# Performance work log

Measured on AMD Instinct MI355X. Metric: run time of the kernel, lower is better.

Reference implementation:

```python
import jax, jax.numpy as jnp
import numpy as np

B, T, D = 2, 2048, 2048
H, LAT, RD = 16, 512, 64
HD = D // H  # 128


def _rope_tables(rd, max_t, theta=10000.0):
    freqs = 1.0 / theta ** (np.arange(0, rd, 2, dtype=np.float32) / rd)
    t = np.arange(max_t, dtype=np.float32)
    ang = np.outer(t, freqs)                      # (T, rd/2)
    cos = np.tile(np.cos(ang), (1, 2))            # (T, rd), matches torch .repeat(1,2)
    sin = np.tile(np.sin(ang), (1, 2))
    return jnp.asarray(cos), jnp.asarray(sin)


def _rotate_half(x):
    d = x.shape[-1] // 2
    return jnp.concatenate([-x[..., d:], x[..., :d]], axis=-1)


def _apply_rope(x, cos, sin):
    # x: (B, H, T, rd); cos/sin: (T, rd) broadcast over B, H
    t = x.shape[2]
    return x * cos[:t][None, None] + _rotate_half(x) * sin[:t][None, None]


def setup_inputs() -> dict:
    key = jax.random.key(0)
    ks = jax.random.split(key, 9)
    s = 0.02  # init scale to keep logits sane
    return {
        "x": jax.random.normal(ks[0], (B, T, D), jnp.float32),
        "Wqd": jax.random.normal(ks[1], (D, LAT), jnp.float32) * s,
        "Wqu": jax.random.normal(ks[2], (LAT, D), jnp.float32) * s,
        "Wqr": jax.random.normal(ks[3], (LAT, H * RD), jnp.float32) * s,
        "Wkvd": jax.random.normal(ks[4], (D, LAT), jnp.float32) * s,
        "Wku": jax.random.normal(ks[5], (LAT, D), jnp.float32) * s,
        "Wvu": jax.random.normal(ks[6], (LAT, D), jnp.float32) * s,
        "Wkr": jax.random.normal(ks[7], (D, RD), jnp.float32) * s,
        "Wo": jax.random.normal(ks[8], (D, D), jnp.float32) * s,
    }


def reference(x, Wqd, Wqu, Wqr, Wkvd, Wku, Wvu, Wkr, Wo):
    b, t, d = x.shape
    cos, sin = _rope_tables(RD, t)

    ql = x @ Wqd                                            # (B,T,LAT)
    q = (ql @ Wqu).reshape(b, t, H, HD).transpose(0, 2, 1, 3)      # (B,H,T,hd)
    qr = (ql @ Wqr).reshape(b, t, H, RD).transpose(0, 2, 1, 3)     # (B,H,T,rd)
    qr = _apply_rope(qr, cos, sin)

    ckv = x @ Wkvd                                          # (B,T,LAT)
    k = (ckv @ Wku).reshape(b, t, H, HD).transpose(0, 2, 1, 3)     # (B,H,T,hd)
    v = (ckv @ Wvu).reshape(b, t, H, HD).transpose(0, 2, 1, 3)     # (B,H,T,hd)

    kr = _apply_rope((x @ Wkr)[:, None], cos, sin)[:, 0]    # (B,T,rd), shared over heads

    scale = 1.0 / jnp.sqrt(jnp.float32(HD + RD))
    scores = (jnp.einsum('bhtd,bhsd->bhts', q, k)
              + jnp.einsum('bhtd,bsd->bhts', qr, kr)) * scale       # (B,H,T,T)

    causal = jnp.tril(jnp.ones((t, t), dtype=bool))
    scores = jnp.where(causal[None, None], scores, jnp.float32(-jnp.inf))
    attn = jax.nn.softmax(scores, axis=-1)

    out = jnp.einsum('bhts,bhsd->bhtd', attn, v)            # (B,H,T,hd)
    out = out.transpose(0, 2, 1, 3).reshape(b, t, d)        # (B,T,D)
    return out @ Wo
```

## Files before the change

kernel.cpp:

```cpp
#include <hip/hip_runtime.h>
#include <cmath>

typedef unsigned short ushort;
typedef __bf16 bf16x8 __attribute__((ext_vector_type(8)));
typedef float f32x4 __attribute__((ext_vector_type(4)));
typedef float f32x16 __attribute__((ext_vector_type(16)));
typedef unsigned int uint4v __attribute__((ext_vector_type(4)));
typedef unsigned int u2v __attribute__((ext_vector_type(2)));
typedef unsigned short ushort4v __attribute__((ext_vector_type(4)));

#define BB 2
#define TT 2048
#define DD 2048
#define HH 16
#define LATD 512
#define RDD 64
#define HDD 128
#define BT 4096
#define LDQ 2048
#define LDK 4096
#define LD1 1088

__device__ __forceinline__ ushort f2bf(float f) {
  union { float f; unsigned u; } v; v.f = f;
  return (ushort)((v.u + 0x7fffu + ((v.u >> 16) & 1u)) >> 16);
}
__device__ __forceinline__ float bf2f(ushort u) {
  union { unsigned u; float f; } v; v.u = ((unsigned)u) << 16; return v.f;
}
__device__ __forceinline__ f32x4 f4zero() {
  f32x4 v; v[0] = 0.f; v[1] = 0.f; v[2] = 0.f; v[3] = 0.f; return v;
}
__device__ __forceinline__ unsigned pkbf(float a, float b) {
  unsigned r;
  asm("v_cvt_pk_bf16_f32 %0, %1, %2" : "=v"(r) : "v"(a), "v"(b));
  return r;
}
__device__ __forceinline__ u2v pl32(unsigned a, unsigned b) {
  return __builtin_amdgcn_permlane32_swap(a, b, false, false);
}
__device__ __forceinline__ float xswap32(float v, int hl) {
  union { float f; unsigned u; } a; a.f = v;
  u2v r = pl32(a.u, a.u);
  union { unsigned u; float f; } o; o.u = hl ? r[0] : r[1];
  return o.f;
}

typedef __attribute__((address_space(1))) void g_void;
typedef __attribute__((address_space(3))) void l_void;
__device__ __forceinline__ void gld16(void* lds, const void* g) {
  __builtin_amdgcn_global_load_lds((g_void*)(unsigned long long)g, (l_void*)lds, 16, 0, 0);
}

__global__ void k_cvt(const float* __restrict__ in, ushort* __restrict__ out, int n4) {
  int i = blockIdx.x * 256 + threadIdx.x;
  if (i >= n4) return;
  f32x4 v = *(const f32x4*)(in + (size_t)i * 4);
  ushort4v u;
#pragma unroll
  for (int r = 0; r < 4; ++r) u[r] = f2bf(v[r]);
  *(ushort4v*)(out + (size_t)i * 4) = u;
}

__global__ void k_twall(const float* __restrict__ Wqd, const float* __restrict__ Wkvd,
                        const float* __restrict__ Wkr, const float* __restrict__ Wqu,
                        const float* __restrict__ Wqr, const float* __restrict__ Wku,
                        const float* __restrict__ Wvu, const float* __restrict__ Wo,
                        ushort* __restrict__ w1T, ushort* __restrict__ w2T,
                        ushort* __restrict__ w3T, ushort* __restrict__ woT) {
  __shared__ float t[32][33];
  int bid = blockIdx.x;
  const float* in; ushort* out; int R, C, gx;
  if (bid < 1024)      { in = Wqd;  out = w1T;                          R = 2048; C = 512;  gx = 16; }
  else if (bid < 2048) { in = Wkvd; out = w1T + (size_t)512 * 2048;     R = 2048; C = 512;  gx = 16; bid -= 1024; }
  else if (bid < 2176) { in = Wkr;  out = w1T + (size_t)1024 * 2048;    R = 2048; C = 64;   gx = 2;  bid -= 2048; }
  else if (bid < 3200) { in = Wqu;  out = w2T;                          R = 512;  C = 2048; gx = 64; bid -= 2176; }
  else if (bid < 3712) { in = Wqr;  out = w2T + (size_t)2048 * 512;     R = 512;  C = 1024; gx = 32; bid -= 3200; }
  else if (bid < 4736) { in = Wku;  out = w3T;                          R = 512;  C = 2048; gx = 64; bid -= 3712; }
  else if (bid < 5760) { in = Wvu;  out = w3T + (size_t)2048 * 512;     R = 512;  C = 2048; gx = 64; bid -= 4736; }
  else                 { in = Wo;   out = woT;                          R = 2048; C = 2048; gx = 64; bid -= 5760; }
  int c0 = (bid % gx) * 32, r0 = (bid / gx) * 32;
  int tx = threadIdx.x, ty = threadIdx.y;
#pragma unroll
  for (int i = 0; i < 4; ++i)
    t[ty + i * 8][tx] = in[(size_t)(r0 + ty + i * 8) * C + c0 + tx];
  __syncthreads();
#pragma unroll
  for (int i = 0; i < 4; ++i)
    out[(size_t)(c0 + ty + i * 8) * R + r0 + tx] = f2bf(t[tx][ty + i * 8]);
}

__global__ void k_tables(float* __restrict__ cosT, float* __restrict__ sinT) {
  int i = blockIdx.x * 256 + threadIdx.x;
  int t = i >> 5, jj = i & 31;
  float freq = exp2f(-(float)jj * (13.287712379549449f / 32.0f));
  float ang = (float)t * freq;
  float s, c;
  sincosf(ang, &s, &c);
  cosT[i] = c; sinT[i] = s;
}

__global__ void k_rope(const ushort* __restrict__ in, int in_stride, ushort* __restrict__ out,
                       int lw, const float* __restrict__ cosT, const float* __restrict__ sinT) {
  int idx = blockIdx.x * 256 + threadIdx.x;
  int row = idx >> lw, col = idx & ((1 << lw) - 1);
  int t = row & (TT - 1);
  int j = col & 63, jj = j & 31;
  float c = cosT[t * 32 + jj], s = sinT[t * 32 + jj];
  const ushort* ip = in + (size_t)row * in_stride;
  float xv = bf2f(ip[col]);
  float xp = (j < 32) ? -bf2f(ip[col + 32]) : bf2f(ip[col - 32]);
  out[idx] = f2bf(xv * c + xp * s);
}

__global__ void k_vt(const ushort* __restrict__ in, ushort* __restrict__ out) {
  __shared__ ushort tile[32][33];
  int bh = blockIdx.z, b = bh >> 4, h = bh & 15;
  int t0 = blockIdx.x * 32, d0 = blockIdx.y * 32;
  int tx = threadIdx.x, ty = threadIdx.y;
#pragma unroll
  for (int i = 0; i < 4; ++i)
    tile[ty + i * 8][tx] = in[(size_t)(b * TT + t0 + ty + i * 8) * LDK + h * HDD + d0 + tx];
  __syncthreads();
#pragma unroll
  for (int i = 0; i < 4; ++i)
    out[(size_t)(bh * HDD + d0 + ty + i * 8) * TT + t0 + tx] = tile[tx][ty + i * 8];
}

__global__ void k_ta(const ushort* __restrict__ in, ushort* __restrict__ out) {
  __shared__ ushort tile[32][33];
  int bh = blockIdx.z, b = bh >> 4, h = bh & 15;
  int t0 = blockIdx.x * 32, d0 = blockIdx.y * 32;
  int tx = threadIdx.x, ty = threadIdx.y;
#pragma unroll
  for (int i = 0; i < 4; ++i)
    tile[ty + i * 8][tx] = in[(size_t)(bh * HDD + d0 + ty + i * 8) * TT + t0 + tx];
  __syncthreads();
#pragma unroll
  for (int i = 0; i < 4; ++i)
    out[(size_t)(b * TT + t0 + ty + i * 8) * DD + h * HDD + d0 + tx] = tile[tx][ty + i * 8];
}

template <typename OutT>
__global__ __launch_bounds__(256) void k_gemm(const ushort* __restrict__ A,
                                              const ushort* __restrict__ Bt,
                                              OutT* __restrict__ C,
                                              int M, int N, int K, int lda, int ldc, float alpha) {
  __shared__ __align__(16) ushort As[128 * 64];
  __shared__ __align__(16) ushort Bs[128 * 64];
  int tid = threadIdx.x;
  int lane = tid & 63, wid = tid >> 6;
  int wm = wid >> 1, wn = wid & 1;
  int lo = lane & 15, hi = lane >> 4;
  int m0 = blockIdx.y * 128, n0 = blockIdx.x * 128;
  int lr = lane >> 3, lc = (lane & 7) * 8;
  f32x4 acc[4][4];
#pragma unroll
  for (int m = 0; m < 4; ++m)
#pragma unroll
    for (int n = 0; n < 4; ++n) acc[m][n] = f4zero();

  for (int k0 = 0; k0 < K; k0 += 64) {
    __syncthreads();
#pragma unroll
    for (int it = 0; it < 4; ++it) {
      int c = wid * 4 + it;
      int row = c * 8 + lr;
      gld16(As + c * 512, A + (size_t)(m0 + row) * lda + k0 + lc);
      gld16(Bs + c * 512, Bt + (size_t)(n0 + row) * K + k0 + lc);
    }
    __syncthreads();
#pragma unroll
    for (int kk = 0; kk < 2; ++kk) {
      bf16x8 af[4], bfr[4];
#pragma unroll
      for (int m = 0; m < 4; ++m)
        af[m] = *(const bf16x8*)(As + (wm * 64 + m * 16 + lo) * 64 + kk * 32 + hi * 8);
#pragma unroll
      for (int n = 0; n < 4; ++n)
        bfr[n] = *(const bf16x8*)(Bs + (wn * 64 + n * 16 + lo) * 64 + kk * 32 + hi * 8);
      __builtin_amdgcn_s_setprio(1);
#pragma unroll
      for (int m = 0; m < 4; ++m)
#pragma unroll
        for (int n = 0; n < 4; ++n)
          acc[m][n] = __builtin_amdgcn_mfma_f32_16x16x32_bf16(af[m], bfr[n], acc[m][n], 0, 0, 0);
      __builtin_amdgcn_s_setprio(0);
    }
  }
#pragma unroll
  for (int m = 0; m < 4; ++m)
#pragma unroll
    for (int n = 0; n < 4; ++n)
#pragma unroll
      for (int r = 0; r < 4; ++r) {
        int row = m0 + wm * 64 + m * 16 + hi * 4 + r;
        int col = n0 + wn * 64 + n * 16 + lo;
        if (col < N) {
          float v = acc[m][n][r] * alpha;
          if constexpr (sizeof(OutT) == 4) C[(size_t)row * ldc + col] = v;
          else C[(size_t)row * ldc + col] = f2bf(v);
        }
      }
}

__global__ __launch_bounds__(256) void k_gemm23(const ushort* __restrict__ A1, const ushort* __restrict__ B1,
                                                ushort* __restrict__ Cq, ushort* __restrict__ Cr,
                                                const ushort* __restrict__ A2, const ushort* __restrict__ B2,
                                                ushort* __restrict__ Ckv, float a1,
                                                const float* __restrict__ cosT, const float* __restrict__ sinT) {
  __shared__ __align__(16) ushort As[128 * 64];
  __shared__ __align__(16) ushort Bs[128 * 64];
  int bx = blockIdx.x;
  const ushort* A; const ushort* Bt; int n0;
  if (bx < 24) { A = A1; Bt = B1; n0 = bx * 128; }
  else         { A = A2; Bt = B2; n0 = (bx - 24) * 128; }
  const int K = LATD, lda = LD1;
  int tid = threadIdx.x;
  int lane = tid & 63, wid = tid >> 6;
  int wm = wid >> 1, wn = wid & 1;
  int lo = lane & 15, hi = lane >> 4;
  int m0 = blockIdx.y * 128;
  int lr = lane >> 3, lc = (lane & 7) * 8;
  f32x4 acc[4][4];
#pragma unroll
  for (int m = 0; m < 4; ++m)
#pragma unroll
    for (int n = 0; n < 4; ++n) acc[m][n] = f4zero();

  for (int k0 = 0; k0 < K; k0 += 64) {
    __syncthreads();
#pragma unroll
    for (int it = 0; it < 4; ++it) {
      int c = wid * 4 + it;
      int row = c * 8 + lr;
      gld16(As + c * 512, A + (size_t)(m0 + row) * lda + k0 + lc);
      gld16(Bs + c * 512, Bt + (size_t)(n0 + row) * K + k0 + lc);
    }
    __syncthreads();
#pragma unroll
    for (int kk = 0; kk < 2; ++kk) {
      bf16x8 af[4], bfr[4];
#pragma unroll
      for (int m = 0; m < 4; ++m)
        af[m] = *(const bf16x8*)(As + (wm * 64 + m * 16 + lo) * 64 + kk * 32 + hi * 8);
#pragma unroll
      for (int n = 0; n < 4; ++n)
        bfr[n] = *(const bf16x8*)(Bs + (wn * 64 + n * 16 + lo) * 64 + kk * 32 + hi * 8);
      __builtin_amdgcn_s_setprio(1);
#pragma unroll
      for (int m = 0; m < 4; ++m)
#pragma unroll
        for (int n = 0; n < 4; ++n)
          acc[m][n] = __builtin_amdgcn_mfma_f32_16x16x32_bf16(af[m], bfr[n], acc[m][n], 0, 0, 0);
      __builtin_amdgcn_s_setprio(0);
    }
  }
  if (bx < 16) {
#pragma unroll
    for (int m = 0; m < 4; ++m)
#pragma unroll
      for (int n = 0; n < 4; ++n)
#pragma unroll
        for (int r = 0; r < 4; ++r) {
          int row = m0 + wm * 64 + m * 16 + hi * 4 + r;
          int col = n0 + wn * 64 + n * 16 + lo;
          Cq[(size_t)row * 2048 + col] = f2bf(acc[m][n][r] * a1);
        }
  } else if (bx < 24) {
#pragma unroll
    for (int m = 0; m < 4; ++m)
#pragma unroll
      for (int r = 0; r < 4; ++r) {
        int row = m0 + wm * 64 + m * 16 + hi * 4 + r;
        int t = row & (TT - 1);
        float c0 = cosT[t * 32 + lo],      s0 = sinT[t * 32 + lo];
        float c1 = cosT[t * 32 + 16 + lo], s1 = sinT[t * 32 + 16 + lo];
        float x0 = acc[m][0][r], x1 = acc[m][1][r];
        float x2 = acc[m][2][r], x3 = acc[m][3][r];
        size_t base = (size_t)row * 1024 + (bx - 16) * 128 + wn * 64 + lo;
        Cr[base +  0] = f2bf((x0 * c0 - x2 * s0) * a1);
        Cr[base + 16] = f2bf((x1 * c1 - x3 * s1) * a1);
        Cr[base + 32] = f2bf((x2 * c0 + x0 * s0) * a1);
        Cr[base + 48] = f2bf((x3 * c1 + x1 * s1) * a1);
      }
  } else {
#pragma unroll
    for (int m = 0; m < 4; ++m)
#pragma unroll
      for (int n = 0; n < 4; ++n)
#pragma unroll
        for (int r = 0; r < 4; ++r) {
          int row = m0 + wm * 64 + m * 16 + hi * 4 + r;
          int col = n0 + wn * 64 + n * 16 + lo;
          Ckv[(size_t)row * 4096 + col] = f2bf(acc[m][n][r]);
        }
  }
}

__global__ __launch_bounds__(256, 2) void k_attn(const ushort* __restrict__ qb, const ushort* __restrict__ qrb,
                                                 const ushort* __restrict__ kb, const ushort* __restrict__ krb,
                                                 const ushort* __restrict__ vt, ushort* __restrict__ aoT) {
  __shared__ __align__(16) ushort KsL[2][64 * 128];
  __shared__ __align__(16) ushort KrL[2][64 * 64];
  const int tid = threadIdx.x, lane = tid & 63, w = tid >> 6;
  const int cq = lane & 31;
  const int hl = lane >> 5;
  const int lin = (int)blockIdx.x + 16 * (int)blockIdx.y + 256 * (int)blockIdx.z;
  const int combo = lin & 31;
  const int pr = lin >> 5, h = combo & 15, b = combo >> 4;
  const int tA = pr, tB = 31 - pr;
  const int nch = tB + 1;
  const int myTile = (w >= 2) ? tB : tA;
  const int myDiag = myTile;
  const int qrow = myTile * 64 + (w & 1) * 32 + cq;
  const int swzK = (cq & 15) << 3;
  const int swzR = (cq & 7) << 3;

  bf16x8 qf[12];
  {
    const ushort* qp = qb + (size_t)(b * TT + qrow) * LDQ + h * HDD;
#pragma unroll
    for (int f = 0; f < 8; ++f) qf[f] = *(const bf16x8*)(qp + f * 16 + hl * 8);
    const ushort* qrp = qrb + (size_t)(b * TT + qrow) * 1024 + h * RDD;
#pragma unroll
    for (int f = 0; f < 4; ++f) qf[8 + f] = *(const bf16x8*)(qrp + f * 16 + hl * 8);
  }
  f32x16 o0, o1, o2, o3;
#pragma unroll
  for (int r = 0; r < 16; ++r) { o0[r] = 0.f; o1[r] = 0.f; o2[r] = 0.f; o3[r] = 0.f; }
  float m = -__builtin_inff(), l = 0.f;

  auto stage = [&](int buf, int kb0) {
#pragma unroll
    for (int it = 0; it < 4; ++it) {
      int cb = (tid & ~63) + it * 256;
      int c = cb + lane;
      int row = c >> 4;
      int ccg = (c & 15) ^ (row & 15);
      gld16(&KsL[buf][cb * 8], kb + (size_t)(b * TT + kb0 + row) * LDK + h * HDD + ccg * 8);
    }
#pragma unroll
    for (int it = 0; it < 2; ++it) {
      int cb = (tid & ~63) + it * 256;
      int c = cb + lane;
      int row = c >> 3;
      int ccg = (c & 7) ^ (row & 7);
      gld16(&KrL[buf][cb * 8], krb + (size_t)(b * TT + kb0 + row) * RDD + ccg * 8);
    }
  };

  stage(0, 0);
  __syncthreads();

  const ushort* vth = vt + (size_t)(b * HH + h) * HDD * TT;

  int cur = 0;
  for (int ch = 0; ch < nch; ++ch) {
    const int kb0 = ch * 64;
    if (ch + 1 < nch) stage(cur ^ 1, kb0 + 64);

    if (ch <= myDiag) {
      f32x16 s0, s1;
#pragma unroll
      for (int r = 0; r < 16; ++r) { s0[r] = 0.f; s1[r] = 0.f; }
      __builtin_amdgcn_s_setprio(1);
#pragma unroll
      for (int f = 0; f < 12; ++f) {
        const ushort* base = (f < 8) ? &KsL[cur][0] : &KrL[cur][0];
        const int stride = (f < 8) ? 128 : 64;
        const int colU = ((f < 8) ? f * 16 : (f - 8) * 16) + hl * 8;
        const int sz = (f < 8) ? swzK : swzR;
        bf16x8 k0 = *(const bf16x8*)(base + cq * stride + (colU ^ sz));
        bf16x8 k1 = *(const bf16x8*)(base + (32 + cq) * stride + (colU ^ sz));
        s0 = __builtin_amdgcn_mfma_f32_32x32x16_bf16(k0, qf[f], s0, 0, 0, 0);
        s1 = __builtin_amdgcn_mfma_f32_32x32x16_bf16(k1, qf[f], s1, 0, 0, 0);
      }
      __builtin_amdgcn_s_setprio(0);

      float mx = -__builtin_inff();
      if (ch == myDiag) {
#pragma unroll
        for (int r = 0; r < 16; ++r) {
          int kp = kb0 + (r & 3) + 8 * (r >> 2) + 4 * hl;
          if (kp > qrow) s0[r] = -__builtin_inff();
          mx = fmaxf(mx, s0[r]);
          if (kp + 32 > qrow) s1[r] = -__builtin_inff();
          mx = fmaxf(mx, s1[r]);
        }
      } else {
#pragma unroll
        for (int r = 0; r < 16; ++r) mx = fmaxf(fmaxf(mx, s0[r]), s1[r]);
      }
      mx = fmaxf(mx, xswap32(mx, hl));

      uint4v va[4], vb2[4];
      {
        const ushort* vp = vth + (size_t)(0 * 32 + cq) * TT + kb0 + hl * 8;
        va[0] = *(const uint4v*)(vp);
        va[1] = *(const uint4v*)(vp + 16);
        va[2] = *(const uint4v*)(vp + 32);
        va[3] = *(const uint4v*)(vp + 48);
      }

      bool defer = __all(mx <= m + 8.f);
      float mnew = defer ? m : fmaxf(m, mx);
      float rs = 0.f;
#pragma unroll
      for (int r = 0; r < 16; ++r) {
        s0[r] = exp2f(s0[r] - mnew); rs += s0[r];
        s1[r] = exp2f(s1[r] - mnew); rs += s1[r];
      }
      rs += xswap32(rs, hl);
      if (!defer) {
        float al = exp2f(m - mnew);
#pragma unroll
        for (int r = 0; r < 16; ++r) { o0[r] *= al; o1[r] *= al; o2[r] *= al; o3[r] *= al; }
        l = l * al + rs;
        m = mnew;
      } else {
        l += rs;
      }

      bf16x8 pf0, pf1, pf2, pf3;
#define PBUILD(PF, S, RB)                                                   \
      {                                                                     \
        unsigned a2 = pkbf(S[RB + 0], S[RB + 1]);                           \
        unsigned b2 = pkbf(S[RB + 2], S[RB + 3]);                           \
        unsigned c2 = pkbf(S[RB + 4], S[RB + 5]);                           \
        unsigned d2 = pkbf(S[RB + 6], S[RB + 7]);                           \
        u2v r02 = pl32(a2, c2);                                             \
        u2v r13 = pl32(b2, d2);                                             \
        union { uint4v u; bf16x8 v; } pb_;                                  \
        pb_.u[0] = r02[0];                                                  \
        pb_.u[1] = r13[0];                                                  \
        pb_.u[2] = r02[1];                                                  \
        pb_.u[3] = r13[1];                                                  \
        PF = pb_.v;                                                         \
      }
      PBUILD(pf0, s0, 0)
      PBUILD(pf1, s0, 8)
      PBUILD(pf2, s1, 0)
      PBUILD(pf3, s1, 8)
#undef PBUILD

#define VLOAD(DST, DT)                                                      \
      {                                                                     \
        const ushort* vp = vth + (size_t)((DT) * 32 + cq) * TT + kb0 + hl * 8;\
        DST[0] = *(const uint4v*)(vp);                                      \
        DST[1] = *(const uint4v*)(vp + 16);                                 \
        DST[2] = *(const uint4v*)(vp + 32);                                 \
        DST[3] = *(const uint4v*)(vp + 48);                                 \
      }
#define PVSTEP(OD, VS)                                                      \
      {                                                                     \
        union { uint4v u; bf16x8 v; } cv_;                                  \
        __builtin_amdgcn_s_setprio(1);                                      \
        cv_.u = VS[0]; OD = __builtin_amdgcn_mfma_f32_32x32x16_bf16(cv_.v, pf0, OD, 0, 0, 0); \
        cv_.u = VS[1]; OD = __builtin_amdgcn_mfma_f32_32x32x16_bf16(cv_.v, pf1, OD, 0, 0, 0); \
        cv_.u = VS[2]; OD = __builtin_amdgcn_mfma_f32_32x32x16_bf16(cv_.v, pf2, OD, 0, 0, 0); \
        cv_.u = VS[3]; OD = __builtin_amdgcn_mfma_f32_32x32x16_bf16(cv_.v, pf3, OD, 0, 0, 0); \
        __builtin_amdgcn_s_setprio(0);                                      \
      }
      VLOAD(vb2, 1)
      PVSTEP(o0, va)
      VLOAD(va, 2)
      PVSTEP(o1, vb2)
      VLOAD(vb2, 3)
      PVSTEP(o2, va)
      PVSTEP(o3, vb2)
#undef VLOAD
#undef PVSTEP
    }

    __syncthreads();
    cur ^= 1;
  }

  float inv = 1.0f / l;
  const size_t obase = (size_t)(b * HH + h) * HDD;
#define OSTORE(OD, DT)                                                      \
  _Pragma("unroll")                                                         \
  for (int r = 0; r < 16; ++r) {                                            \
    int dr = (DT) * 32 + (r & 3) + 8 * (r >> 2) + 4 * hl;                   \
    aoT[(obase + dr) * TT + qrow] = f2bf(OD[r] * inv);                      \
  }
  OSTORE(o0, 0)
  OSTORE(o1, 1)
  OSTORE(o2, 2)
  OSTORE(o3, 3)
#undef OSTORE
}

extern "C" void kernel_launch(void* const* d_in, const int* in_sizes, int n_in,
                              void* d_out, int out_size, void* d_ws, size_t ws_size,
                              hipStream_t stream) {
  (void)in_sizes; (void)n_in; (void)out_size; (void)ws_size;
  const float* x    = (const float*)d_in[0];
  const float* Wqd  = (const float*)d_in[1];
  const float* Wqu  = (const float*)d_in[2];
  const float* Wqr  = (const float*)d_in[3];
  const float* Wkvd = (const float*)d_in[4];
  const float* Wku  = (const float*)d_in[5];
  const float* Wvu  = (const float*)d_in[6];
  const float* Wkr  = (const float*)d_in[7];
  const float* Wo   = (const float*)d_in[8];
  float* out = (float*)d_out;

  char* ws = (char*)d_ws;
  size_t off = 0;
  auto alloc = [&](size_t bytes) { void* p = ws + off; off += (bytes + 255) & ~(size_t)255; return p; };
  ushort* xb   = (ushort*)alloc((size_t)BT * DD * 2);
  ushort* w1T  = (ushort*)alloc((size_t)(LD1 + 64) * DD * 2);
  ushort* w2T  = (ushort*)alloc((size_t)3072 * LATD * 2);
  ushort* w3T  = (ushort*)alloc((size_t)4096 * LATD * 2);
  ushort* woT  = (ushort*)alloc((size_t)DD * DD * 2);
  ushort* xc   = (ushort*)alloc((size_t)BT * LD1 * 2);
  ushort* qqr  = (ushort*)alloc((size_t)BT * 2048 * 2);
  ushort* kv   = (ushort*)alloc((size_t)BT * 4096 * 2);
  ushort* qrB  = (ushort*)alloc((size_t)BT * 1024 * 2);
  ushort* krB  = (ushort*)alloc((size_t)BT * RDD * 2);
  ushort* vtB  = (ushort*)alloc((size_t)BT * DD * 2);
  ushort* aoB  = (ushort*)alloc((size_t)BT * DD * 2);
  float*  cosT = (float*)alloc((size_t)TT * 32 * 4);
  float*  sinT = (float*)alloc((size_t)TT * 32 * 4);
  ushort* aoT  = xb;

  float qscale = 1.4426950408889634f / sqrtf(192.0f);

  k_cvt<<<BT * DD / 4 / 256, 256, 0, stream>>>(x, xb, BT * DD / 4);
  k_twall<<<dim3(9856), dim3(32, 8), 0, stream>>>(Wqd, Wkvd, Wkr, Wqu, Wqr, Wku, Wvu, Wo,
                                                  w1T, w2T, w3T, woT);
  k_tables<<<TT * 32 / 256, 256, 0, stream>>>(cosT, sinT);

  k_gemm<ushort><<<dim3(9, BT / 128), 256, 0, stream>>>(xb, w1T, xc, BT, LD1, DD, DD, LD1, 1.0f);
  k_gemm23<<<dim3(56, BT / 128), 256, 0, stream>>>(xc, w2T, qqr, qrB, xc + 512, w3T, kv,
                                                   qscale, cosT, sinT);

  k_rope<<<BT * RDD / 256, 256, 0, stream>>>(xc + 1024, LD1, krB, 6, cosT, sinT);
  k_vt<<<dim3(TT / 32, HDD / 32, BB * HH), dim3(32, 8), 0, stream>>>(kv + 2048, vtB);

  k_attn<<<dim3(16, HH, BB), 256, 0, stream>>>(qqr, qrB, kv, krB, vtB, aoT);
  k_ta<<<dim3(TT / 32, HDD / 32, BB * HH), dim3(32, 8), 0, stream>>>(aoT, aoB);

  k_gemm<float><<<dim3(16, BT / 128), 256, 0, stream>>>(aoB, woT, out, BT, DD, DD, DD, DD, 1.0f);
}
```

Measured before the change: 300.6 us.

## Merge prep kernels, fuse key RoPE into GEMM1 epilogue, write attention output row-major

The conversion, weight-transpose and RoPE-table kernels are merged into one prep launch. The key-RoPE pass moves into the epilogue of the first projection GEMM, so the kr columns are rotated in registers and never round-trip through memory. The attention kernel now stages its output through its shared-memory buffer and writes row-major (B,T,D) directly, which removes the separate transpose kernel. This cuts launches and global traffic, but adds LDS reuse and epilogue complexity in the attention and GEMM kernels.

```diff
diff --git a/kernel.cpp b/kernel.cpp
--- a/kernel.cpp
+++ b/kernel.cpp
@@ -52,24 +52,36 @@
   __builtin_amdgcn_global_load_lds((g_void*)(unsigned long long)g, (l_void*)lds, 16, 0, 0);
 }
 
-__global__ void k_cvt(const float* __restrict__ in, ushort* __restrict__ out, int n4) {
-  int i = blockIdx.x * 256 + threadIdx.x;
-  if (i >= n4) return;
-  f32x4 v = *(const f32x4*)(in + (size_t)i * 4);
-  ushort4v u;
-#pragma unroll
-  for (int r = 0; r < 4; ++r) u[r] = f2bf(v[r]);
-  *(ushort4v*)(out + (size_t)i * 4) = u;
-}
-
-__global__ void k_twall(const float* __restrict__ Wqd, const float* __restrict__ Wkvd,
-                        const float* __restrict__ Wkr, const float* __restrict__ Wqu,
-                        const float* __restrict__ Wqr, const float* __restrict__ Wku,
-                        const float* __restrict__ Wvu, const float* __restrict__ Wo,
-                        ushort* __restrict__ w1T, ushort* __restrict__ w2T,
-                        ushort* __restrict__ w3T, ushort* __restrict__ woT) {
+__global__ void k_prep(const float* __restrict__ x, ushort* __restrict__ xb,
+                       float* __restrict__ cosT, float* __restrict__ sinT,
+                       const float* __restrict__ Wqd, const float* __restrict__ Wkvd,
+                       const float* __restrict__ Wkr, const float* __restrict__ Wqu,
+                       const float* __restrict__ Wqr, const float* __restrict__ Wku,
+                       const float* __restrict__ Wvu, const float* __restrict__ Wo,
+                       ushort* __restrict__ w1T, ushort* __restrict__ w2T,
+                       ushort* __restrict__ w3T, ushort* __restrict__ woT) {
   __shared__ float t[32][33];
-  int bid = blockIdx.x;
+  int bid = blockIdx.x, tid = threadIdx.x;
+  if (bid < 8192) {
+    int i = bid * 256 + tid;
+    f32x4 v = *(const f32x4*)(x + (size_t)i * 4);
+    ushort4v u;
+#pragma unroll
+    for (int r = 0; r < 4; ++r) u[r] = f2bf(v[r]);
+    *(ushort4v*)(xb + (size_t)i * 4) = u;
+    return;
+  }
+  if (bid < 8448) {
+    int i = (bid - 8192) * 256 + tid;
+    int tt = i >> 5, jj = i & 31;
+    float freq = exp2f(-(float)jj * (13.287712379549449f / 32.0f));
+    float ang = (float)tt * freq;
+    float s, c;
+    sincosf(ang, &s, &c);
+    cosT[i] = c; sinT[i] = s;
+    return;
+  }
+  bid -= 8448;
   const float* in; ushort* out; int R, C, gx;
   if (bid < 1024)      { in = Wqd;  out = w1T;                          R = 2048; C = 512;  gx = 16; }
   else if (bid < 2048) { in = Wkvd; out = w1T + (size_t)512 * 2048;     R = 2048; C = 512;  gx = 16; bid -= 1024; }
@@ -80,7 +92,7 @@
   else if (bid < 5760) { in = Wvu;  out = w3T + (size_t)2048 * 512;     R = 512;  C = 2048; gx = 64; bid -= 4736; }
   else                 { in = Wo;   out = woT;                          R = 2048; C = 2048; gx = 64; bid -= 5760; }
   int c0 = (bid % gx) * 32, r0 = (bid / gx) * 32;
-  int tx = threadIdx.x, ty = threadIdx.y;
+  int tx = tid & 31, ty = tid >> 5;
 #pragma unroll
   for (int i = 0; i < 4; ++i)
     t[ty + i * 8][tx] = in[(size_t)(r0 + ty + i * 8) * C + c0 + tx];
@@ -88,29 +100,6 @@
 #pragma unroll
   for (int i = 0; i < 4; ++i)
     out[(size_t)(c0 + ty + i * 8) * R + r0 + tx] = f2bf(t[tx][ty + i * 8]);
-}
-
-__global__ void k_tables(float* __restrict__ cosT, float* __restrict__ sinT) {
-  int i = blockIdx.x * 256 + threadIdx.x;
-  int t = i >> 5, jj = i & 31;
-  float freq = exp2f(-(float)jj * (13.287712379549449f / 32.0f));
-  float ang = (float)t * freq;
-  float s, c;
-  sincosf(ang, &s, &c);
-  cosT[i] = c; sinT[i] = s;
-}
-
-__global__ void k_rope(const ushort* __restrict__ in, int in_stride, ushort* __restrict__ out,
-                       int lw, const float* __restrict__ cosT, const float* __restrict__ sinT) {
-  int idx = blockIdx.x * 256 + threadIdx.x;
-  int row = idx >> lw, col = idx & ((1 << lw) - 1);
-  int t = row & (TT - 1);
-  int j = col & 63, jj = j & 31;
-  float c = cosT[t * 32 + jj], s = sinT[t * 32 + jj];
-  const ushort* ip = in + (size_t)row * in_stride;
-  float xv = bf2f(ip[col]);
-  float xp = (j < 32) ? -bf2f(ip[col + 32]) : bf2f(ip[col - 32]);
-  out[idx] = f2bf(xv * c + xp * s);
 }
 
 __global__ void k_vt(const ushort* __restrict__ in, ushort* __restrict__ out) {
@@ -125,20 +114,6 @@
 #pragma unroll
   for (int i = 0; i < 4; ++i)
     out[(size_t)(bh * HDD + d0 + ty + i * 8) * TT + t0 + tx] = tile[tx][ty + i * 8];
-}
-
-__global__ void k_ta(const ushort* __restrict__ in, ushort* __restrict__ out) {
-  __shared__ ushort tile[32][33];
-  int bh = blockIdx.z, b = bh >> 4, h = bh & 15;
-  int t0 = blockIdx.x * 32, d0 = blockIdx.y * 32;
-  int tx = threadIdx.x, ty = threadIdx.y;
-#pragma unroll
-  for (int i = 0; i < 4; ++i)
-    tile[ty + i * 8][tx] = in[(size_t)(bh * HDD + d0 + ty + i * 8) * TT + t0 + tx];
-  __syncthreads();
-#pragma unroll
-  for (int i = 0; i < 4; ++i)
-    out[(size_t)(b * TT + t0 + ty + i * 8) * DD + h * HDD + d0 + tx] = tile[tx][ty + i * 8];
 }
 
 template <typename OutT>
@@ -202,6 +177,84 @@
           else C[(size_t)row * ldc + col] = f2bf(v);
         }
       }
+}
+
+__global__ __launch_bounds__(256) void k_gemm1(const ushort* __restrict__ A, const ushort* __restrict__ Bt,
+                                               ushort* __restrict__ C, ushort* __restrict__ Kr,
+                                               const float* __restrict__ cosT, const float* __restrict__ sinT) {
+  __shared__ __align__(16) ushort As[128 * 64];
+  __shared__ __align__(16) ushort Bs[128 * 64];
+  const int K = DD, lda = DD, ldc = LD1;
+  int tid = threadIdx.x;
+  int lane = tid & 63, wid = tid >> 6;
+  int wm = wid >> 1, wn = wid & 1;
+  int lo = lane & 15, hi = lane >> 4;
+  int m0 = blockIdx.y * 128, n0 = blockIdx.x * 128;
+  int bx = blockIdx.x;
+  int lr = lane >> 3, lc = (lane & 7) * 8;
+  f32x4 acc[4][4];
+#pragma unroll
+  for (int m = 0; m < 4; ++m)
+#pragma unroll
+    for (int n = 0; n < 4; ++n) acc[m][n] = f4zero();
+
+  for (int k0 = 0; k0 < K; k0 += 64) {
+    __syncthreads();
+#pragma unroll
+    for (int it = 0; it < 4; ++it) {
+      int c = wid * 4 + it;
+      int row = c * 8 + lr;
+      gld16(As + c * 512, A + (size_t)(m0 + row) * lda + k0 + lc);
+      gld16(Bs + c * 512, Bt + (size_t)(n0 + row) * K + k0 + lc);
+    }
+    __syncthreads();
+#pragma unroll
+    for (int kk = 0; kk < 2; ++kk) {
+      bf16x8 af[4], bfr[4];
+#pragma unroll
+      for (int m = 0; m < 4; ++m)
+        af[m] = *(const bf16x8*)(As + (wm * 64 + m * 16 + lo) * 64 + kk * 32 + hi * 8);
+#pragma unroll
+      for (int n = 0; n < 4; ++n)
+        bfr[n] = *(const bf16x8*)(Bs + (wn * 64 + n * 16 + lo) * 64 + kk * 32 + hi * 8);
+      __builtin_amdgcn_s_setprio(1);
+#pragma unroll
+      for (int m = 0; m < 4; ++m)
+#pragma unroll
+        for (int n = 0; n < 4; ++n)
+          acc[m][n] = __builtin_amdgcn_mfma_f32_16x16x32_bf16(af[m], bfr[n], acc[m][n], 0, 0, 0);
+      __builtin_amdgcn_s_setprio(0);
+    }
+  }
+  if (bx < 8) {
+#pragma unroll
+    for (int m = 0; m < 4; ++m)
+#pragma unroll
+      for (int n = 0; n < 4; ++n)
+#pragma unroll
+        for (int r = 0; r < 4; ++r) {
+          int row = m0 + wm * 64 + m * 16 + hi * 4 + r;
+          int col = n0 + wn * 64 + n * 16 + lo;
+          C[(size_t)row * ldc + col] = f2bf(acc[m][n][r]);
+        }
+  } else if (wn == 0) {
+#pragma unroll
+    for (int m = 0; m < 4; ++m)
+#pragma unroll
+      for (int r = 0; r < 4; ++r) {
+        int row = m0 + wm * 64 + m * 16 + hi * 4 + r;
+        int t = row & (TT - 1);
+        float c0 = cosT[t * 32 + lo],      s0 = sinT[t * 32 + lo];
+        float c1 = cosT[t * 32 + 16 + lo], s1 = sinT[t * 32 + 16 + lo];
+        float x0 = acc[m][0][r], x1 = acc[m][1][r];
+        float x2 = acc[m][2][r], x3 = acc[m][3][r];
+        size_t base = (size_t)row * 64 + lo;
+        Kr[base +  0] = f2bf(x0 * c0 - x2 * s0);
+        Kr[base + 16] = f2bf(x1 * c1 - x3 * s1);
+        Kr[base + 32] = f2bf(x2 * c0 + x0 * s0);
+        Kr[base + 48] = f2bf(x3 * c1 + x1 * s1);
+      }
+  }
 }
 
 __global__ __launch_bounds__(256) void k_gemm23(const ushort* __restrict__ A1, const ushort* __restrict__ B1,
@@ -300,9 +353,10 @@
 
 __global__ __launch_bounds__(256, 2) void k_attn(const ushort* __restrict__ qb, const ushort* __restrict__ qrb,
                                                  const ushort* __restrict__ kb, const ushort* __restrict__ krb,
-                                                 const ushort* __restrict__ vt, ushort* __restrict__ aoT) {
-  __shared__ __align__(16) ushort KsL[2][64 * 128];
-  __shared__ __align__(16) ushort KrL[2][64 * 64];
+                                                 const ushort* __restrict__ vt, ushort* __restrict__ ao) {
+  __shared__ __align__(16) ushort SH[24576];
+#define KS(buf) (SH + (buf) * 8192)
+#define KR(buf) (SH + 16384 + (buf) * 4096)
   const int tid = threadIdx.x, lane = tid & 63, w = tid >> 6;
   const int cq = lane & 31;
   const int hl = lane >> 5;
@@ -338,7 +392,7 @@
       int c = cb + lane;
       int row = c >> 4;
       int ccg = (c & 15) ^ (row & 15);
-      gld16(&KsL[buf][cb * 8], kb + (size_t)(b * TT + kb0 + row) * LDK + h * HDD + ccg * 8);
+      gld16(&KS(buf)[cb * 8], kb + (size_t)(b * TT + kb0 + row) * LDK + h * HDD + ccg * 8);
     }
 #pragma unroll
     for (int it = 0; it < 2; ++it) {
@@ -346,7 +400,7 @@
       int c = cb + lane;
       int row = c >> 3;
       int ccg = (c & 7) ^ (row & 7);
-      gld16(&KrL[buf][cb * 8], krb + (size_t)(b * TT + kb0 + row) * RDD + ccg * 8);
+      gld16(&KR(buf)[cb * 8], krb + (size_t)(b * TT + kb0 + row) * RDD + ccg * 8);
     }
   };
 
@@ -367,7 +421,7 @@
       __builtin_amdgcn_s_setprio(1);
 #pragma unroll
       for (int f = 0; f < 12; ++f) {
-        const ushort* base = (f < 8) ? &KsL[cur][0] : &KrL[cur][0];
+        const ushort* base = (f < 8) ? KS(cur) : KR(cur);
         const int stride = (f < 8) ? 128 : 64;
         const int colU = ((f < 8) ? f * 16 : (f - 8) * 16) + hl * 8;
         const int sz = (f < 8) ? swzK : swzR;
@@ -478,18 +532,31 @@
   }
 
   float inv = 1.0f / l;
-  const size_t obase = (size_t)(b * HH + h) * HDD;
-#define OSTORE(OD, DT)                                                      \
+  const int ebase = w * 4352;
+#define OSPILL(OD, DT)                                                      \
   _Pragma("unroll")                                                         \
-  for (int r = 0; r < 16; ++r) {                                            \
-    int dr = (DT) * 32 + (r & 3) + 8 * (r >> 2) + 4 * hl;                   \
-    aoT[(obase + dr) * TT + qrow] = f2bf(OD[r] * inv);                      \
-  }
-  OSTORE(o0, 0)
-  OSTORE(o1, 1)
-  OSTORE(o2, 2)
-  OSTORE(o3, 3)
-#undef OSTORE
+  for (int g = 0; g < 4; ++g) {                                             \
+    ushort4v u;                                                             \
+    _Pragma("unroll")                                                       \
+    for (int j = 0; j < 4; ++j) u[j] = f2bf(OD[g * 4 + j] * inv);           \
+    *(ushort4v*)(&SH[ebase + cq * 136 + (DT) * 32 + g * 8 + hl * 4]) = u;   \
+  }
+  OSPILL(o0, 0)
+  OSPILL(o1, 1)
+  OSPILL(o2, 2)
+  OSPILL(o3, 3)
+#undef OSPILL
+  {
+    const size_t rbase = (size_t)(b * TT + myTile * 64 + (w & 1) * 32);
+#pragma unroll
+    for (int p = 0; p < 8; ++p) {
+      int q = p * 4 + (lane >> 4);
+      uint4v v = *(const uint4v*)(&SH[ebase + q * 136 + (lane & 15) * 8]);
+      *(uint4v*)(&ao[(rbase + q) * DD + h * HDD + (lane & 15) * 8]) = v;
+    }
+  }
+#undef KS
+#undef KR
 }
 
 extern "C" void kernel_launch(void* const* d_in, const int* in_sizes, int n_in,
@@ -524,24 +591,20 @@
   ushort* aoB  = (ushort*)alloc((size_t)BT * DD * 2);
   float*  cosT = (float*)alloc((size_t)TT * 32 * 4);
   float*  sinT = (float*)alloc((size_t)TT * 32 * 4);
-  ushort* aoT  = xb;
 
   float qscale = 1.4426950408889634f / sqrtf(192.0f);
 
-  k_cvt<<<BT * DD / 4 / 256, 256, 0, stream>>>(x, xb, BT * DD / 4);
-  k_twall<<<dim3(9856), dim3(32, 8), 0, stream>>>(Wqd, Wkvd, Wkr, Wqu, Wqr, Wku, Wvu, Wo,
-                                                  w1T, w2T, w3T, woT);
-  k_tables<<<TT * 32 / 256, 256, 0, stream>>>(cosT, sinT);
-
-  k_gemm<ushort><<<dim3(9, BT / 128), 256, 0, stream>>>(xb, w1T, xc, BT, LD1, DD, DD, LD1, 1.0f);
+  k_prep<<<dim3(18304), 256, 0, stream>>>(x, xb, cosT, sinT,
+                                          Wqd, Wkvd, Wkr, Wqu, Wqr, Wku, Wvu, Wo,
+                                          w1T, w2T, w3T, woT);
+
+  k_gemm1<<<dim3(9, BT / 128), 256, 0, stream>>>(xb, w1T, xc, krB, cosT, sinT);
   k_gemm23<<<dim3(56, BT / 128), 256, 0, stream>>>(xc, w2T, qqr, qrB, xc + 512, w3T, kv,
                                                    qscale, cosT, sinT);
 
-  k_rope<<<BT * RDD / 256, 256, 0, stream>>>(xc + 1024, LD1, krB, 6, cosT, sinT);
   k_vt<<<dim3(TT / 32, HDD / 32, BB * HH), dim3(32, 8), 0, stream>>>(kv + 2048, vtB);
 
-  k_attn<<<dim3(16, HH, BB), 256, 0, stream>>>(qqr, qrB, kv, krB, vtB, aoT);
-  k_ta<<<dim3(TT / 32, HDD / 32, BB * HH), dim3(32, 8), 0, stream>>>(aoT, aoB);
+  k_attn<<<dim3(16, HH, BB), 256, 0, stream>>>(qqr, qrB, kv, krB, vtB, aoB);
 
   k_gemm<float><<<dim3(16, BT / 128), 256, 0, stream>>>(aoB, woT, out, BT, DD, DD, DD, DD, 1.0f);
 }
```

New measurement: 282.7 us. 1.06x faster.
